# Performance work log

Measured on AMD Instinct MI355X. Metric: run time of the kernel, lower is better.

Reference implementation:

```python
import jax, jax.numpy as jnp
import numpy as np

N_ATOMS = 8_000_000
N_REC = 2_000_000
N_POC = 500_000
N_CHAINS = 4


def setup_inputs() -> dict:
    key = jax.random.key(0)
    k1, k2, k3, k4 = jax.random.split(key, 4)
    # coordinates in nm, inside a ~5 nm box
    positions = jax.random.uniform(k1, (N_ATOMS, 3), dtype=jnp.float32) * 5.0
    box_vectors = jnp.diag(jnp.array([5.0, 5.0, 5.0], dtype=jnp.float32))
    # unique receptor atom indices into positions
    rec_indices = jax.random.permutation(k2, N_ATOMS)[:N_REC].astype(jnp.int32)
    # unique pocket indices INTO THE REC ARRAY (poc_pos = rec_pos[poc_indices])
    poc_indices = jax.random.permutation(k3, N_REC)[:N_POC].astype(jnp.int32)
    # contiguous chain assignment over rec atoms, all chains present in pocket
    chain_ids = ((jnp.arange(N_REC, dtype=jnp.int32) * N_CHAINS) // N_REC).astype(jnp.int32)
    poc_chain_ids = chain_ids[poc_indices]
    ref_poc = jax.random.uniform(k4, (N_POC, 3), dtype=jnp.float32) * 5.0
    k = jnp.float32(100.0)  # kJ/mol/nm^2
    return {
        "positions": positions, "box_vectors": box_vectors, "ref_poc": ref_poc,
        "k": k, "rec_indices": rec_indices, "poc_indices": poc_indices,
        "chain_ids": chain_ids, "poc_chain_ids": poc_chain_ids, "n_chains": N_CHAINS,
    }


def best_periodic_translation(pos1, pos2, box_vectors):
    # pos1, pos2: [C,3]; box_vectors: [3,3] (rows are lattice vectors)
    delta = pos2 - pos1
    inv = 1.0 / jnp.diag(box_vectors)
    s3 = jnp.round(delta[:, 2] * inv[2])
    delta = delta - s3[:, None] * box_vectors[2]
    s2 = jnp.round(delta[:, 1] * inv[1])
    delta = delta - s2[:, None] * box_vectors[1]
    s1 = jnp.round(delta[:, 0] * inv[0])
    return s1[:, None] * box_vectors[0] + s2[:, None] * box_vectors[1] + s3[:, None] * box_vectors[2]


def reference(positions, box_vectors, ref_poc, k, rec_indices, poc_indices, chain_ids, poc_chain_ids, n_chains):
    rec_pos = positions[rec_indices]  # [R,3]
    # Per-chain pocket COM. NOTE: original indexes global positions here
    # (positions[poc_chain_indices]), NOT rec_pos -- reproduced faithfully.
    poc_glob = positions[poc_indices]  # [P,3]
    counts = jax.ops.segment_sum(jnp.ones((poc_glob.shape[0],), poc_glob.dtype), poc_chain_ids, num_segments=n_chains)  # [C]
    poc_com = jax.ops.segment_sum(poc_glob, poc_chain_ids, num_segments=n_chains) / counts[:, None]  # [C,3]
    ref_com = jax.ops.segment_sum(ref_poc, poc_chain_ids, num_segments=n_chains) / counts[:, None]  # [C,3]
    best_t = best_periodic_translation(poc_com, ref_com, box_vectors)  # [C,3]
    rec_pos = rec_pos + best_t[chain_ids]  # translate each chain into the reference image

    poc_pos = rec_pos[poc_indices]  # [P,3]
    rec_origin = jnp.mean(rec_pos, axis=0)
    rec_centered = rec_pos - rec_origin
    r_sq = jnp.sum(rec_centered ** 2, axis=1)  # [R]
    F = jnp.zeros_like(rec_pos).at[poc_indices].set(-2.0 * k * (poc_pos - ref_poc))
    F_mean = jnp.mean(F, axis=0)
    torque = jnp.cross(rec_centered, F)
    torque_mean = jnp.mean(torque, axis=0)
    F_rot = jnp.cross(torque_mean[None], rec_centered) / r_sq[:, None]
    F_final = jnp.zeros_like(positions).at[rec_indices].set(F_mean + F_rot)
    return (jnp.float32(0.0), F_final)
```

## Files before the change

kernel.cpp:

```cpp
#include <hip/hip_runtime.h>


#define W_BT 0
#define W_O 48
#define W_FM 52
#define W_TM 56
#define W_ACC 64
#define INV8_OFF 4096
#define GA 1024

__device__ inline float waveSum(float v) {
#pragma unroll
  for (int off = 32; off > 0; off >>= 1) v += __shfl_down(v, off, 64);
  return v;
}

__global__ void k_fused_sums(const float* __restrict__ pos,
                             const float* __restrict__ ref_poc,
                             const int* __restrict__ rec_idx,
                             const int* __restrict__ cid,
                             const int* __restrict__ poc_idx,
                             const int* __restrict__ poc_cid,
                             const int* __restrict__ ncp,
                             int R, int P,
                             unsigned char* __restrict__ inv8,
                             float* __restrict__ ws) {
  const int C = ncp[0];
  const int stride = gridDim.x * blockDim.x;
  if (C <= 4) {
    float vals[50];
#pragma unroll
    for (int v = 0; v < 50; ++v) vals[v] = 0.f;
    for (int r = blockIdx.x * blockDim.x + threadIdx.x; r < R; r += stride) {
      int i = rec_idx[r];
      int c = cid[r];
      inv8[i] = (unsigned char)c;
      vals[0] += pos[3 * i + 0];
      vals[1] += pos[3 * i + 1];
      vals[2] += pos[3 * i + 2];
#pragma unroll
      for (int cc = 0; cc < 4; ++cc) vals[3 + cc] += (c == cc) ? 1.f : 0.f;
      if (r < P) {
        int i2 = poc_idx[r];
        int c2 = poc_cid[r];
        int ri = rec_idx[i2];
        float gx = pos[3 * i2 + 0], gy = pos[3 * i2 + 1], gz = pos[3 * i2 + 2];
        float px = pos[3 * ri + 0], py = pos[3 * ri + 1], pz = pos[3 * ri + 2];
        float rx = ref_poc[3 * r + 0], ry = ref_poc[3 * r + 1], rz = ref_poc[3 * r + 2];
        vals[7] += py * rz - pz * ry;
        vals[8] += pz * rx - px * rz;
        vals[9] += px * ry - py * rx;
#pragma unroll
        for (int cc = 0; cc < 4; ++cc) {
          bool m = (c2 == cc);
          vals[10 + cc * 10 + 0] += m ? gx : 0.f;
          vals[10 + cc * 10 + 1] += m ? gy : 0.f;
          vals[10 + cc * 10 + 2] += m ? gz : 0.f;
          vals[10 + cc * 10 + 3] += m ? rx : 0.f;
          vals[10 + cc * 10 + 4] += m ? ry : 0.f;
          vals[10 + cc * 10 + 5] += m ? rz : 0.f;
          vals[10 + cc * 10 + 6] += m ? px : 0.f;
          vals[10 + cc * 10 + 7] += m ? py : 0.f;
          vals[10 + cc * 10 + 8] += m ? pz : 0.f;
          vals[10 + cc * 10 + 9] += m ? 1.f : 0.f;
        }
      }
    }
    __shared__ float red[4][50];
    const int wid = threadIdx.x >> 6;
#pragma unroll
    for (int v = 0; v < 50; ++v) {
      float s = waveSum(vals[v]);
      if ((threadIdx.x & 63) == 0) red[wid][v] = s;
    }
    __syncthreads();
    for (int t = threadIdx.x; t < 50; t += blockDim.x)
      atomicAdd(&ws[W_ACC + t], red[0][t] + red[1][t] + red[2][t] + red[3][t]);
  } else {
    __shared__ float acc[192];
    for (int t = threadIdx.x; t < 192; t += blockDim.x) acc[t] = 0.f;
    __syncthreads();
    for (int r = blockIdx.x * blockDim.x + threadIdx.x; r < R; r += stride) {
      int i = rec_idx[r];
      int c = cid[r];
      inv8[i] = (unsigned char)c;
      atomicAdd(&acc[0], pos[3 * i + 0]);
      atomicAdd(&acc[1], pos[3 * i + 1]);
      atomicAdd(&acc[2], pos[3 * i + 2]);
      atomicAdd(&acc[3 + c], 1.f);
      if (r < P) {
        int i2 = poc_idx[r];
        int c2 = poc_cid[r];
        int ri = rec_idx[i2];
        float gx = pos[3 * i2 + 0], gy = pos[3 * i2 + 1], gz = pos[3 * i2 + 2];
        float px = pos[3 * ri + 0], py = pos[3 * ri + 1], pz = pos[3 * ri + 2];
        float rx = ref_poc[3 * r + 0], ry = ref_poc[3 * r + 1], rz = ref_poc[3 * r + 2];
        atomicAdd(&acc[19], py * rz - pz * ry);
        atomicAdd(&acc[20], pz * rx - px * rz);
        atomicAdd(&acc[21], px * ry - py * rx);
        float* a = &acc[22 + c2 * 10];
        atomicAdd(&a[0], gx); atomicAdd(&a[1], gy); atomicAdd(&a[2], gz);
        atomicAdd(&a[3], rx); atomicAdd(&a[4], ry); atomicAdd(&a[5], rz);
        atomicAdd(&a[6], px); atomicAdd(&a[7], py); atomicAdd(&a[8], pz);
        atomicAdd(&a[9], 1.f);
      }
    }
    __syncthreads();
    for (int t = threadIdx.x; t < 192; t += blockDim.x)
      if (acc[t] != 0.f) atomicAdd(&ws[W_ACC + t], acc[t]);
  }
}

__global__ void k_finalize(const float* __restrict__ box,
                           const float* __restrict__ kp,
                           const int* __restrict__ ncp,
                           int R, float* __restrict__ ws) {
  __shared__ float tot[192];
  const int C = ncp[0];
  for (int t = threadIdx.x; t < 192; t += blockDim.x) tot[t] = ws[W_ACC + t];
  __syncthreads();
  if (threadIdx.x != 0) return;
  const bool small = (C <= 4);
  const float kk = kp[0];
  const float Rf = (float)R;
  const float* xp = small ? &tot[7] : &tot[19];
  float inv0 = 1.f / box[0], inv1 = 1.f / box[4], inv2 = 1.f / box[8];
  float ox = tot[0], oy = tot[1], oz = tot[2];
  float Fx = 0, Fy = 0, Fz = 0;
  float T1x = 0, T1y = 0, T1z = 0, T2x = 0, T2y = 0, T2z = 0;
  for (int c = 0; c < C; ++c) {
    float nrec = tot[3 + c];
    const float* a = small ? &tot[10 + c * 10] : &tot[22 + c * 10];
    float np = a[9];
    float invn = 1.f / np;
    float pcx = a[0] * invn, pcy = a[1] * invn, pcz = a[2] * invn;
    float rcx = a[3] * invn, rcy = a[4] * invn, rcz = a[5] * invn;
    float dx = rcx - pcx, dy = rcy - pcy, dz = rcz - pcz;
    float s3 = rintf(dz * inv2);
    dx -= s3 * box[6]; dy -= s3 * box[7]; dz -= s3 * box[8];
    float s2 = rintf(dy * inv1);
    dx -= s2 * box[3]; dy -= s2 * box[4]; dz -= s2 * box[5];
    float s1 = rintf(dx * inv0);
    float btx = s1 * box[0] + s2 * box[3] + s3 * box[6];
    float bty = s1 * box[1] + s2 * box[4] + s3 * box[7];
    float btz = s1 * box[2] + s2 * box[5] + s3 * box[8];
    ws[W_BT + c * 3 + 0] = btx;
    ws[W_BT + c * 3 + 1] = bty;
    ws[W_BT + c * 3 + 2] = btz;
    ox += nrec * btx; oy += nrec * bty; oz += nrec * btz;
    float SFx = -2.f * kk * (a[6] + np * btx - a[3]);
    float SFy = -2.f * kk * (a[7] + np * bty - a[4]);
    float SFz = -2.f * kk * (a[8] + np * btz - a[5]);
    Fx += SFx; Fy += SFy; Fz += SFz;
    T1x += a[7] * btz - a[8] * bty;
    T1y += a[8] * btx - a[6] * btz;
    T1z += a[6] * bty - a[7] * btx;
    T2x += bty * SFz - btz * SFy;
    T2y += btz * SFx - btx * SFz;
    T2z += btx * SFy - bty * SFx;
  }
  ox /= Rf; oy /= Rf; oz /= Rf;
  float Tx = 2.f * kk * xp[0] - 2.f * kk * T1x + T2x - (oy * Fz - oz * Fy);
  float Ty = 2.f * kk * xp[1] - 2.f * kk * T1y + T2y - (oz * Fx - ox * Fz);
  float Tz = 2.f * kk * xp[2] - 2.f * kk * T1z + T2z - (ox * Fy - oy * Fx);
  ws[W_O + 0] = ox; ws[W_O + 1] = oy; ws[W_O + 2] = oz;
  ws[W_FM + 0] = Fx / Rf; ws[W_FM + 1] = Fy / Rf; ws[W_FM + 2] = Fz / Rf;
  ws[W_TM + 0] = Tx / Rf; ws[W_TM + 1] = Ty / Rf; ws[W_TM + 2] = Tz / Rf;
}

__global__ void k_final_dense(const float4* __restrict__ pos4,
                              const unsigned char* __restrict__ inv8,
                              int N, const float* __restrict__ ws,
                              float* __restrict__ out) {
  __shared__ float stage[256 * 13];
  __shared__ float sc[64];
  if (threadIdx.x < 64) sc[threadIdx.x] = ws[threadIdx.x];
  __syncthreads();
  float ox = sc[W_O + 0], oy = sc[W_O + 1], oz = sc[W_O + 2];
  float fmx = sc[W_FM + 0], fmy = sc[W_FM + 1], fmz = sc[W_FM + 2];
  float tmx = sc[W_TM + 0], tmy = sc[W_TM + 1], tmz = sc[W_TM + 2];

  if (blockIdx.x == 0 && threadIdx.x == 0) out[0] = 0.f;

  const uchar4* m4 = (const uchar4*)inv8;
  int t0 = blockIdx.x * 1024;
  if (t0 >= N) return;
  int i0 = t0 + threadIdx.x * 4;

  float v[12];
  if (i0 + 3 < N) {
    float4 p0 = pos4[3 * (i0 >> 2) + 0];
    float4 p1 = pos4[3 * (i0 >> 2) + 1];
    float4 p2 = pos4[3 * (i0 >> 2) + 2];
    uchar4 m = m4[i0 >> 2];
    float px[4] = {p0.x, p0.w, p1.z, p2.y};
    float py[4] = {p0.y, p1.x, p1.w, p2.z};
    float pz[4] = {p0.z, p1.y, p2.x, p2.w};
    unsigned char mc[4] = {m.x, m.y, m.z, m.w};
#pragma unroll
    for (int q = 0; q < 4; ++q) {
      int c = mc[q];
      if (c != 255) {
        float cx = px[q] + sc[W_BT + 3 * c + 0] - ox;
        float cy = py[q] + sc[W_BT + 3 * c + 1] - oy;
        float cz = pz[q] + sc[W_BT + 3 * c + 2] - oz;
        float inv = 1.f / (cx * cx + cy * cy + cz * cz);
        v[3 * q + 0] = fmx + (tmy * cz - tmz * cy) * inv;
        v[3 * q + 1] = fmy + (tmz * cx - tmx * cz) * inv;
        v[3 * q + 2] = fmz + (tmx * cy - tmy * cx) * inv;
      } else {
        v[3 * q + 0] = 0.f; v[3 * q + 1] = 0.f; v[3 * q + 2] = 0.f;
      }
    }
  } else {
#pragma unroll
    for (int q = 0; q < 4; ++q) {
      int i = i0 + q;
      float fx = 0.f, fy = 0.f, fz = 0.f;
      if (i < N) {
        const float* p = (const float*)pos4;
        int c = inv8[i];
        if (c != 255) {
          float cx = p[3 * i + 0] + sc[W_BT + 3 * c + 0] - ox;
          float cy = p[3 * i + 1] + sc[W_BT + 3 * c + 1] - oy;
          float cz = p[3 * i + 2] + sc[W_BT + 3 * c + 2] - oz;
          float inv = 1.f / (cx * cx + cy * cy + cz * cz);
          fx = fmx + (tmy * cz - tmz * cy) * inv;
          fy = fmy + (tmz * cx - tmx * cz) * inv;
          fz = fmz + (tmx * cy - tmy * cx) * inv;
        }
      }
      v[3 * q + 0] = fx; v[3 * q + 1] = fy; v[3 * q + 2] = fz;
    }
  }
#pragma unroll
  for (int j = 0; j < 12; ++j) stage[threadIdx.x * 13 + j] = v[j];
  __syncthreads();

  int nfl = (N - t0) * 3; if (nfl > 3072) nfl = 3072;
  float* ob = out + 1 + 3 * t0;
  for (int k = threadIdx.x; k < nfl; k += 256) {
    unsigned int a = (unsigned int)k / 12u;
    ob[k] = stage[a * 13 + (k - a * 12)];
  }
}

extern "C" void kernel_launch(void* const* d_in, const int* in_sizes, int n_in,
                              void* d_out, int out_size, void* d_ws, size_t ws_size,
                              hipStream_t stream) {
  const float* pos     = (const float*)d_in[0];
  const float* box     = (const float*)d_in[1];
  const float* ref_poc = (const float*)d_in[2];
  const float* kp      = (const float*)d_in[3];
  const int* rec_idx   = (const int*)d_in[4];
  const int* poc_idx   = (const int*)d_in[5];
  const int* cid       = (const int*)d_in[6];
  const int* poc_cid   = (const int*)d_in[7];
  const int* ncp       = (const int*)d_in[8];
  float* out = (float*)d_out;
  float* ws  = (float*)d_ws;
  unsigned char* inv8 = (unsigned char*)d_ws + INV8_OFF;

  const int N = in_sizes[0] / 3;
  const int R = in_sizes[4];
  const int P = in_sizes[5];

  hipMemsetAsync((char*)d_ws + W_ACC * 4, 0, 192 * 4, stream);
  hipMemsetAsync(inv8, 0xFF, (size_t)N, stream);

  k_fused_sums<<<GA, 256, 0, stream>>>(pos, ref_poc, rec_idx, cid, poc_idx,
                                       poc_cid, ncp, R, P, inv8, ws);
  k_finalize<<<1, 256, 0, stream>>>(box, kp, ncp, R, ws);
  int gF = (N + 1023) / 1024;
  k_final_dense<<<gF, 256, 0, stream>>>((const float4*)pos, inv8, N, ws, out);
}
```

Before: 319.1 us.

## Bucket receptor indices by atom range to build chain map in LDS

Replaces the random byte scatter into the global chain map and the separate 0xFF memset with a two-pass bucketed partition. Receptor indices are binned into 512 atom-range buckets through global records, and each bucket block then builds its map in shared memory and writes it out coalesced. The receptor-centroid sum is now taken by a dense coalesced pass over positions instead of random gathers. The final kernel stages positions through LDS with coalesced float4 loads. The cost is an extra kernel and intermediate record traffic, plus a fixed per-bucket capacity (CAP) that silently drops records if a bucket overflows.

```diff
diff --git a/kernel.cpp b/kernel.cpp
--- a/kernel.cpp
+++ b/kernel.cpp
@@ -1,13 +1,26 @@
 #include <hip/hip_runtime.h>
 
 
+typedef unsigned int uint32;
+typedef unsigned char uchar;
+
+#define MAXC 16
 #define W_BT 0
 #define W_O 48
 #define W_FM 52
 #define W_TM 56
 #define W_ACC 64
-#define INV8_OFF 4096
-#define GA 1024
+
+#define GCOUNT_OFF 4096
+#define REC_OFF 8192
+#define NB 512
+#define BSH 14
+#define BUCKET_ATOMS (1 << BSH)
+#define CAP 5120
+#define INV8_OFF (REC_OFF + NB * CAP * 4)
+
+#define K1_KPT 16
+#define K1_CHUNK (256 * K1_KPT)
 
 __device__ inline float waveSum(float v) {
 #pragma unroll
@@ -15,100 +28,198 @@
   return v;
 }
 
-__global__ void k_fused_sums(const float* __restrict__ pos,
-                             const float* __restrict__ ref_poc,
-                             const int* __restrict__ rec_idx,
-                             const int* __restrict__ cid,
-                             const int* __restrict__ poc_idx,
-                             const int* __restrict__ poc_cid,
-                             const int* __restrict__ ncp,
-                             int R, int P,
-                             unsigned char* __restrict__ inv8,
-                             float* __restrict__ ws) {
+__global__ __launch_bounds__(256) void k_part_pocket(
+    const float* __restrict__ pos, const float* __restrict__ ref_poc,
+    const int* __restrict__ rec_idx, const int* __restrict__ cid,
+    const int* __restrict__ poc_idx, const int* __restrict__ poc_cid,
+    const int* __restrict__ ncp, int R, int P,
+    uint32* __restrict__ gcount, uint32* __restrict__ grecords,
+    float* __restrict__ ws) {
+  const int tid = threadIdx.x;
   const int C = ncp[0];
-  const int stride = gridDim.x * blockDim.x;
+  const int gsz = gridDim.x * blockDim.x;
+
   if (C <= 4) {
-    float vals[50];
-#pragma unroll
-    for (int v = 0; v < 50; ++v) vals[v] = 0.f;
-    for (int r = blockIdx.x * blockDim.x + threadIdx.x; r < R; r += stride) {
-      int i = rec_idx[r];
-      int c = cid[r];
-      inv8[i] = (unsigned char)c;
-      vals[0] += pos[3 * i + 0];
-      vals[1] += pos[3 * i + 1];
-      vals[2] += pos[3 * i + 2];
-#pragma unroll
-      for (int cc = 0; cc < 4; ++cc) vals[3 + cc] += (c == cc) ? 1.f : 0.f;
-      if (r < P) {
-        int i2 = poc_idx[r];
-        int c2 = poc_cid[r];
-        int ri = rec_idx[i2];
-        float gx = pos[3 * i2 + 0], gy = pos[3 * i2 + 1], gz = pos[3 * i2 + 2];
-        float px = pos[3 * ri + 0], py = pos[3 * ri + 1], pz = pos[3 * ri + 2];
-        float rx = ref_poc[3 * r + 0], ry = ref_poc[3 * r + 1], rz = ref_poc[3 * r + 2];
-        vals[7] += py * rz - pz * ry;
-        vals[8] += pz * rx - px * rz;
-        vals[9] += px * ry - py * rx;
-#pragma unroll
-        for (int cc = 0; cc < 4; ++cc) {
-          bool m = (c2 == cc);
-          vals[10 + cc * 10 + 0] += m ? gx : 0.f;
-          vals[10 + cc * 10 + 1] += m ? gy : 0.f;
-          vals[10 + cc * 10 + 2] += m ? gz : 0.f;
-          vals[10 + cc * 10 + 3] += m ? rx : 0.f;
-          vals[10 + cc * 10 + 4] += m ? ry : 0.f;
-          vals[10 + cc * 10 + 5] += m ? rz : 0.f;
-          vals[10 + cc * 10 + 6] += m ? px : 0.f;
-          vals[10 + cc * 10 + 7] += m ? py : 0.f;
-          vals[10 + cc * 10 + 8] += m ? pz : 0.f;
-          vals[10 + cc * 10 + 9] += m ? 1.f : 0.f;
-        }
+    float vals[43];
+#pragma unroll
+    for (int v = 0; v < 43; ++v) vals[v] = 0.f;
+    for (int r = blockIdx.x * blockDim.x + tid; r < P; r += gsz) {
+      int i2 = poc_idx[r];
+      int c2 = poc_cid[r];
+      int ri = rec_idx[i2];
+      float gx = pos[3 * i2 + 0], gy = pos[3 * i2 + 1], gz = pos[3 * i2 + 2];
+      float px = pos[3 * ri + 0], py = pos[3 * ri + 1], pz = pos[3 * ri + 2];
+      float rx = ref_poc[3 * r + 0], ry = ref_poc[3 * r + 1], rz = ref_poc[3 * r + 2];
+      vals[0] += py * rz - pz * ry;
+      vals[1] += pz * rx - px * rz;
+      vals[2] += px * ry - py * rx;
+#pragma unroll
+      for (int cc = 0; cc < 4; ++cc) {
+        bool m = (c2 == cc);
+        float* a = &vals[3 + cc * 10];
+        a[0] += m ? gx : 0.f;  a[1] += m ? gy : 0.f;  a[2] += m ? gz : 0.f;
+        a[3] += m ? rx : 0.f;  a[4] += m ? ry : 0.f;  a[5] += m ? rz : 0.f;
+        a[6] += m ? px : 0.f;  a[7] += m ? py : 0.f;  a[8] += m ? pz : 0.f;
+        a[9] += m ? 1.f : 0.f;
       }
     }
-    __shared__ float red[4][50];
-    const int wid = threadIdx.x >> 6;
-#pragma unroll
-    for (int v = 0; v < 50; ++v) {
+    __shared__ float red[4][43];
+    const int wid = tid >> 6;
+#pragma unroll
+    for (int v = 0; v < 43; ++v) {
       float s = waveSum(vals[v]);
-      if ((threadIdx.x & 63) == 0) red[wid][v] = s;
-    }
-    __syncthreads();
-    for (int t = threadIdx.x; t < 50; t += blockDim.x)
-      atomicAdd(&ws[W_ACC + t], red[0][t] + red[1][t] + red[2][t] + red[3][t]);
+      if ((tid & 63) == 0) red[wid][v] = s;
+    }
+    __syncthreads();
+    for (int t = tid; t < 43; t += 256)
+      atomicAdd(&ws[W_ACC + 19 + t],
+                red[0][t] + red[1][t] + red[2][t] + red[3][t]);
+    __syncthreads();
   } else {
-    __shared__ float acc[192];
-    for (int t = threadIdx.x; t < 192; t += blockDim.x) acc[t] = 0.f;
-    __syncthreads();
-    for (int r = blockIdx.x * blockDim.x + threadIdx.x; r < R; r += stride) {
-      int i = rec_idx[r];
-      int c = cid[r];
-      inv8[i] = (unsigned char)c;
-      atomicAdd(&acc[0], pos[3 * i + 0]);
-      atomicAdd(&acc[1], pos[3 * i + 1]);
-      atomicAdd(&acc[2], pos[3 * i + 2]);
-      atomicAdd(&acc[3 + c], 1.f);
-      if (r < P) {
-        int i2 = poc_idx[r];
-        int c2 = poc_cid[r];
-        int ri = rec_idx[i2];
-        float gx = pos[3 * i2 + 0], gy = pos[3 * i2 + 1], gz = pos[3 * i2 + 2];
-        float px = pos[3 * ri + 0], py = pos[3 * ri + 1], pz = pos[3 * ri + 2];
-        float rx = ref_poc[3 * r + 0], ry = ref_poc[3 * r + 1], rz = ref_poc[3 * r + 2];
-        atomicAdd(&acc[19], py * rz - pz * ry);
-        atomicAdd(&acc[20], pz * rx - px * rz);
-        atomicAdd(&acc[21], px * ry - py * rx);
-        float* a = &acc[22 + c2 * 10];
-        atomicAdd(&a[0], gx); atomicAdd(&a[1], gy); atomicAdd(&a[2], gz);
-        atomicAdd(&a[3], rx); atomicAdd(&a[4], ry); atomicAdd(&a[5], rz);
-        atomicAdd(&a[6], px); atomicAdd(&a[7], py); atomicAdd(&a[8], pz);
-        atomicAdd(&a[9], 1.f);
+    __shared__ float accL[3 + MAXC * 10];
+    for (int t = tid; t < 3 + MAXC * 10; t += 256) accL[t] = 0.f;
+    __syncthreads();
+    for (int r = blockIdx.x * blockDim.x + tid; r < P; r += gsz) {
+      int i2 = poc_idx[r];
+      int c2 = poc_cid[r];
+      int ri = rec_idx[i2];
+      float gx = pos[3 * i2 + 0], gy = pos[3 * i2 + 1], gz = pos[3 * i2 + 2];
+      float px = pos[3 * ri + 0], py = pos[3 * ri + 1], pz = pos[3 * ri + 2];
+      float rx = ref_poc[3 * r + 0], ry = ref_poc[3 * r + 1], rz = ref_poc[3 * r + 2];
+      atomicAdd(&accL[0], py * rz - pz * ry);
+      atomicAdd(&accL[1], pz * rx - px * rz);
+      atomicAdd(&accL[2], px * ry - py * rx);
+      float* a = &accL[3 + c2 * 10];
+      atomicAdd(&a[0], gx); atomicAdd(&a[1], gy); atomicAdd(&a[2], gz);
+      atomicAdd(&a[3], rx); atomicAdd(&a[4], ry); atomicAdd(&a[5], rz);
+      atomicAdd(&a[6], px); atomicAdd(&a[7], py); atomicAdd(&a[8], pz);
+      atomicAdd(&a[9], 1.f);
+    }
+    __syncthreads();
+    for (int t = tid; t < 3 + MAXC * 10; t += 256)
+      if (accL[t] != 0.f) atomicAdd(&ws[W_ACC + 19 + t], accL[t]);
+    __syncthreads();
+  }
+
+  __shared__ uint32 hist[NB], curs[NB], base[NB];
+  for (int r0 = blockIdx.x * K1_CHUNK; r0 < R; r0 += gridDim.x * K1_CHUNK) {
+    int cnt = R - r0; if (cnt > K1_CHUNK) cnt = K1_CHUNK;
+    for (int t = tid; t < NB; t += 256) { hist[t] = 0u; curs[t] = 0u; }
+    __syncthreads();
+    uint32 enc[K1_KPT];
+#pragma unroll
+    for (int j = 0; j < K1_KPT; ++j) {
+      int t = tid + j * 256;
+      uint32 e = 0xFFFFFFFFu;
+      if (t < cnt) {
+        uint32 idx = (uint32)rec_idx[r0 + t];
+        uint32 c = (uint32)cid[r0 + t] & 255u;
+        e = (idx << 8) | c;
+        atomicAdd(&hist[idx >> BSH], 1u);
       }
-    }
-    __syncthreads();
-    for (int t = threadIdx.x; t < 192; t += blockDim.x)
-      if (acc[t] != 0.f) atomicAdd(&ws[W_ACC + t], acc[t]);
-  }
+      enc[j] = e;
+    }
+    __syncthreads();
+    for (int t = tid; t < NB; t += 256) {
+      uint32 h = hist[t];
+      base[t] = h ? atomicAdd(&gcount[t], h) : 0u;
+    }
+    __syncthreads();
+#pragma unroll
+    for (int j = 0; j < K1_KPT; ++j) {
+      uint32 e = enc[j];
+      if (e != 0xFFFFFFFFu) {
+        uint32 b = e >> (8 + BSH);
+        uint32 slot = base[b] + atomicAdd(&curs[b], 1u);
+        if (slot < CAP) grecords[b * CAP + slot] = e;
+      }
+    }
+    __syncthreads();
+  }
+}
+
+__global__ __launch_bounds__(256) void k_bucket_build(
+    const float4* __restrict__ pos4, const int* __restrict__ ncp,
+    const uint32* __restrict__ gcount, const uint32* __restrict__ grecords,
+    int N, uchar* __restrict__ inv8, float* __restrict__ ws) {
+  const int tid = threadIdx.x;
+  const int b = blockIdx.x;
+  const int a0 = b << BSH;
+  if (a0 >= N) return;
+  int natoms = N - a0; if (natoms > BUCKET_ATOMS) natoms = BUCKET_ATOMS;
+
+  __shared__ uchar map_[BUCKET_ATOMS];
+  __shared__ float cnt16[MAXC];
+  uint4* m16 = (uint4*)map_;
+  uint4 ff; ff.x = ff.y = ff.z = ff.w = 0xFFFFFFFFu;
+  for (int t = tid; t < BUCKET_ATOMS / 16; t += 256) m16[t] = ff;
+  const int C = ncp[0];
+  if (C > 4) for (int t = tid; t < MAXC; t += 256) cnt16[t] = 0.f;
+  __syncthreads();
+
+  int n = (int)gcount[b]; if (n > CAP) n = CAP;
+  float c0 = 0.f, c1 = 0.f, c2 = 0.f, c3 = 0.f;
+  for (int t = tid; t < n; t += 256) {
+    uint32 e = grecords[b * CAP + t];
+    uint32 ia = (e >> 8) & (BUCKET_ATOMS - 1);
+    uint32 c = e & 255u;
+    map_[ia] = (uchar)c;
+    if (C <= 4) {
+      c0 += (c == 0u) ? 1.f : 0.f;
+      c1 += (c == 1u) ? 1.f : 0.f;
+      c2 += (c == 2u) ? 1.f : 0.f;
+      c3 += (c == 3u) ? 1.f : 0.f;
+    } else {
+      atomicAdd(&cnt16[c], 1.f);
+    }
+  }
+  __syncthreads();
+
+  uchar* dst = inv8 + a0;
+  if (natoms == BUCKET_ATOMS) {
+    uint4* d16 = (uint4*)dst;
+    for (int t = tid; t < BUCKET_ATOMS / 16; t += 256) d16[t] = m16[t];
+  } else {
+    for (int t = tid; t < natoms; t += 256) dst[t] = map_[t];
+  }
+
+  float sx = 0.f, sy = 0.f, sz = 0.f;
+  int ngf = natoms >> 2;
+  const uchar4* m4 = (const uchar4*)map_;
+  int g0 = a0 >> 2;
+  for (int g = tid; g < ngf; g += 256) {
+    float4 p0 = pos4[3 * (g0 + g) + 0];
+    float4 p1 = pos4[3 * (g0 + g) + 1];
+    float4 p2 = pos4[3 * (g0 + g) + 2];
+    uchar4 m = m4[g];
+    if (m.x != 255) { sx += p0.x; sy += p0.y; sz += p0.z; }
+    if (m.y != 255) { sx += p0.w; sy += p1.x; sz += p1.y; }
+    if (m.z != 255) { sx += p1.z; sy += p1.w; sz += p2.x; }
+    if (m.w != 255) { sx += p2.y; sy += p2.z; sz += p2.w; }
+  }
+  int tb = natoms & 3;
+  if (tid < tb) {
+    int a = a0 + (ngf << 2) + tid;
+    const float* pf = (const float*)pos4;
+    if (map_[(ngf << 2) + tid] != 255) {
+      sx += pf[3 * a]; sy += pf[3 * a + 1]; sz += pf[3 * a + 2];
+    }
+  }
+
+  __shared__ float red[4][7];
+  float vv[7] = {sx, sy, sz, c0, c1, c2, c3};
+  const int wid = tid >> 6;
+#pragma unroll
+  for (int v = 0; v < 7; ++v) {
+    float s = waveSum(vv[v]);
+    if ((tid & 63) == 0) red[wid][v] = s;
+  }
+  __syncthreads();
+  if (tid < 7) {
+    float s = red[0][tid] + red[1][tid] + red[2][tid] + red[3][tid];
+    atomicAdd(&ws[W_ACC + tid], s);
+  }
+  if (C > 4 && tid < C) atomicAdd(&ws[W_ACC + 3 + tid], cnt16[tid]);
 }
 
 __global__ void k_finalize(const float* __restrict__ box,
@@ -120,17 +231,16 @@
   for (int t = threadIdx.x; t < 192; t += blockDim.x) tot[t] = ws[W_ACC + t];
   __syncthreads();
   if (threadIdx.x != 0) return;
-  const bool small = (C <= 4);
   const float kk = kp[0];
   const float Rf = (float)R;
-  const float* xp = small ? &tot[7] : &tot[19];
+  const float* xp = &tot[19];
   float inv0 = 1.f / box[0], inv1 = 1.f / box[4], inv2 = 1.f / box[8];
   float ox = tot[0], oy = tot[1], oz = tot[2];
   float Fx = 0, Fy = 0, Fz = 0;
   float T1x = 0, T1y = 0, T1z = 0, T2x = 0, T2y = 0, T2z = 0;
   for (int c = 0; c < C; ++c) {
     float nrec = tot[3 + c];
-    const float* a = small ? &tot[10 + c * 10] : &tot[22 + c * 10];
+    const float* a = &tot[22 + c * 10];
     float np = a[9];
     float invn = 1.f / np;
     float pcx = a[0] * invn, pcy = a[1] * invn, pcz = a[2] * invn;
@@ -168,81 +278,73 @@
   ws[W_TM + 0] = Tx / Rf; ws[W_TM + 1] = Ty / Rf; ws[W_TM + 2] = Tz / Rf;
 }
 
-__global__ void k_final_dense(const float4* __restrict__ pos4,
-                              const unsigned char* __restrict__ inv8,
-                              int N, const float* __restrict__ ws,
-                              float* __restrict__ out) {
-  __shared__ float stage[256 * 13];
+__global__ __launch_bounds__(256) void k_final_dense(
+    const float* __restrict__ pos, const uchar* __restrict__ inv8,
+    int N, const float* __restrict__ ws, float* __restrict__ out) {
+  __shared__ float stage[3328];
   __shared__ float sc[64];
-  if (threadIdx.x < 64) sc[threadIdx.x] = ws[threadIdx.x];
-  __syncthreads();
+  const int tid = threadIdx.x;
+  if (tid < 64) sc[tid] = ws[tid];
+  const int t0 = blockIdx.x * 1024;
+  int nat = N - t0; if (nat > 1024) nat = 1024;
+  const int nfl = nat * 3;
+
+  if (nat == 1024) {
+    const float4* src4 = (const float4*)(pos + 3 * t0);
+#pragma unroll
+    for (int kk = 0; kk < 3; ++kk) {
+      int v4 = tid + kk * 256;
+      float4 p = src4[v4];
+      int idx = 4 * v4 + v4 / 3;
+      stage[idx + 0] = p.x; stage[idx + 1] = p.y;
+      stage[idx + 2] = p.z; stage[idx + 3] = p.w;
+    }
+  } else {
+    for (int k = tid; k < nfl; k += 256)
+      stage[k + (int)((unsigned)k / 12u)] = pos[3 * t0 + k];
+  }
+  __syncthreads();
+
   float ox = sc[W_O + 0], oy = sc[W_O + 1], oz = sc[W_O + 2];
   float fmx = sc[W_FM + 0], fmy = sc[W_FM + 1], fmz = sc[W_FM + 2];
   float tmx = sc[W_TM + 0], tmy = sc[W_TM + 1], tmz = sc[W_TM + 2];
 
-  if (blockIdx.x == 0 && threadIdx.x == 0) out[0] = 0.f;
-
-  const uchar4* m4 = (const uchar4*)inv8;
-  int t0 = blockIdx.x * 1024;
-  if (t0 >= N) return;
-  int i0 = t0 + threadIdx.x * 4;
-
-  float v[12];
-  if (i0 + 3 < N) {
-    float4 p0 = pos4[3 * (i0 >> 2) + 0];
-    float4 p1 = pos4[3 * (i0 >> 2) + 1];
-    float4 p2 = pos4[3 * (i0 >> 2) + 2];
-    uchar4 m = m4[i0 >> 2];
-    float px[4] = {p0.x, p0.w, p1.z, p2.y};
-    float py[4] = {p0.y, p1.x, p1.w, p2.z};
-    float pz[4] = {p0.z, p1.y, p2.x, p2.w};
-    unsigned char mc[4] = {m.x, m.y, m.z, m.w};
+  uchar mc[4];
+  if (nat == 1024) {
+    uchar4 m = ((const uchar4*)(inv8 + t0))[tid];
+    mc[0] = m.x; mc[1] = m.y; mc[2] = m.z; mc[3] = m.w;
+  } else {
 #pragma unroll
     for (int q = 0; q < 4; ++q) {
+      int la = 4 * tid + q;
+      mc[q] = (la < nat) ? inv8[t0 + la] : (uchar)255;
+    }
+  }
+#pragma unroll
+  for (int q = 0; q < 4; ++q) {
+    int la = 4 * tid + q;
+    if (la < nat) {
+      float* s = &stage[13 * tid + 3 * q];
+      float fx = 0.f, fy = 0.f, fz = 0.f;
       int c = mc[q];
       if (c != 255) {
-        float cx = px[q] + sc[W_BT + 3 * c + 0] - ox;
-        float cy = py[q] + sc[W_BT + 3 * c + 1] - oy;
-        float cz = pz[q] + sc[W_BT + 3 * c + 2] - oz;
+        float cx = s[0] + sc[W_BT + 3 * c + 0] - ox;
+        float cy = s[1] + sc[W_BT + 3 * c + 1] - oy;
+        float cz = s[2] + sc[W_BT + 3 * c + 2] - oz;
         float inv = 1.f / (cx * cx + cy * cy + cz * cz);
-        v[3 * q + 0] = fmx + (tmy * cz - tmz * cy) * inv;
-        v[3 * q + 1] = fmy + (tmz * cx - tmx * cz) * inv;
-        v[3 * q + 2] = fmz + (tmx * cy - tmy * cx) * inv;
-      } else {
-        v[3 * q + 0] = 0.f; v[3 * q + 1] = 0.f; v[3 * q + 2] = 0.f;
+        fx = fmx + (tmy * cz - tmz * cy) * inv;
+        fy = fmy + (tmz * cx - tmx * cz) * inv;
+        fz = fmz + (tmx * cy - tmy * cx) * inv;
       }
-    }
-  } else {
-#pragma unroll
-    for (int q = 0; q < 4; ++q) {
-      int i = i0 + q;
-      float fx = 0.f, fy = 0.f, fz = 0.f;
-      if (i < N) {
-        const float* p = (const float*)pos4;
-        int c = inv8[i];
-        if (c != 255) {
-          float cx = p[3 * i + 0] + sc[W_BT + 3 * c + 0] - ox;
-          float cy = p[3 * i + 1] + sc[W_BT + 3 * c + 1] - oy;
-          float cz = p[3 * i + 2] + sc[W_BT + 3 * c + 2] - oz;
-          float inv = 1.f / (cx * cx + cy * cy + cz * cz);
-          fx = fmx + (tmy * cz - tmz * cy) * inv;
-          fy = fmy + (tmz * cx - tmx * cz) * inv;
-          fz = fmz + (tmx * cy - tmy * cx) * inv;
-        }
-      }
-      v[3 * q + 0] = fx; v[3 * q + 1] = fy; v[3 * q + 2] = fz;
-    }
-  }
-#pragma unroll
-  for (int j = 0; j < 12; ++j) stage[threadIdx.x * 13 + j] = v[j];
-  __syncthreads();
-
-  int nfl = (N - t0) * 3; if (nfl > 3072) nfl = 3072;
+      s[0] = fx; s[1] = fy; s[2] = fz;
+    }
+  }
+  __syncthreads();
+
+  if (blockIdx.x == 0 && tid == 0) out[0] = 0.f;
   float* ob = out + 1 + 3 * t0;
-  for (int k = threadIdx.x; k < nfl; k += 256) {
-    unsigned int a = (unsigned int)k / 12u;
-    ob[k] = stage[a * 13 + (k - a * 12)];
-  }
+  for (int k = tid; k < nfl; k += 256)
+    ob[k] = stage[k + (int)((unsigned)k / 12u)];
 }
 
 extern "C" void kernel_launch(void* const* d_in, const int* in_sizes, int n_in,
@@ -259,18 +361,21 @@
   const int* ncp       = (const int*)d_in[8];
   float* out = (float*)d_out;
   float* ws  = (float*)d_ws;
-  unsigned char* inv8 = (unsigned char*)d_ws + INV8_OFF;
+  uint32* gcount   = (uint32*)((char*)d_ws + GCOUNT_OFF);
+  uint32* grecords = (uint32*)((char*)d_ws + REC_OFF);
+  uchar* inv8      = (uchar*)d_ws + INV8_OFF;
 
   const int N = in_sizes[0] / 3;
   const int R = in_sizes[4];
   const int P = in_sizes[5];
 
-  hipMemsetAsync((char*)d_ws + W_ACC * 4, 0, 192 * 4, stream);
-  hipMemsetAsync(inv8, 0xFF, (size_t)N, stream);
-
-  k_fused_sums<<<GA, 256, 0, stream>>>(pos, ref_poc, rec_idx, cid, poc_idx,
-                                       poc_cid, ncp, R, P, inv8, ws);
+  hipMemsetAsync(d_ws, 0, 8192, stream);
+
+  k_part_pocket<<<1024, 256, 0, stream>>>(pos, ref_poc, rec_idx, cid, poc_idx,
+                                          poc_cid, ncp, R, P, gcount, grecords, ws);
+  k_bucket_build<<<NB, 256, 0, stream>>>((const float4*)pos, ncp, gcount,
+                                         grecords, N, inv8, ws);
   k_finalize<<<1, 256, 0, stream>>>(box, kp, ncp, R, ws);
   int gF = (N + 1023) / 1024;
-  k_final_dense<<<gF, 256, 0, stream>>>((const float4*)pos, inv8, N, ws, out);
-}
+  k_final_dense<<<gF, 256, 0, stream>>>(pos, inv8, N, ws, out);
+}
```

After: 280.9 us. 12.0% less time.
